# Performance work log

Hardware: AMD Instinct MI355X
Metric: run time of the kernel (lower is better)

Reference implementation:

```python
import jax, jax.numpy as jnp
import numpy as np

N, E = 50000, 800000
F, H, M = 64, 128, 64  # feature_dim, hidden_dim, message_dim (message_dim must equal feature_dim)


def _mlp(x, W1, b1, W2, b2):
    return jnp.maximum(x @ W1 + b1, 0.0) @ W2 + b2


def setup_inputs() -> dict:
    key = jax.random.key(0)
    ks = jax.random.split(key, 20)
    p = lambda k, s: (jax.random.normal(k, s, jnp.float32) * 0.05)
    return {
        "z_h": jax.random.normal(ks[0], (N, F), jnp.float32),
        "pos_world": jax.random.normal(ks[1], (3,), jnp.float32),
        "edge_index": jax.random.randint(ks[2], (2, E), 0, N),
        "We1": p(ks[3], (2 * F + 8, H)), "be1": p(ks[4], (H,)),
        "We2": p(ks[5], (H, M)), "be2": p(ks[6], (M,)),
        "Wg1": p(ks[7], (2 * F + 8, H)), "bg1": p(ks[8], (H,)),
        "Wg2": p(ks[9], (H, 1)), "bg2": p(ks[10], (1,)),
        "Wn1": p(ks[11], (F + M, H)), "bn1": p(ks[12], (H,)),
        "Wn2": p(ks[13], (H, F)), "bn2": p(ks[14], (F,)),
        "Ww1": p(ks[15], (F + 3, H)), "bw1": p(ks[16], (H,)),
        "Ww2": p(ks[17], (H, M)), "bw2": p(ks[18], (M,)),
    }


def reference(z_h, pos_world, edge_index,
              We1, be1, We2, be2,
              Wg1, bg1, Wg2, bg2,
              Wn1, bn1, Wn2, bn2,
              Ww1, bw1, Ww2, bw2):
    src, tgt = edge_index[0], edge_index[1]
    zs = z_h[src]  # [E, F]
    zt = z_h[tgt]  # [E, F]

    # edge features: diff(3) + dist(1) + vel cross product(3) + its norm(1)
    diff = zs[:, 0:3] - zt[:, 0:3]
    dist = jnp.sum(diff * diff, axis=-1, keepdims=True)
    cross = jnp.cross(zs[:, 3:6], zt[:, 3:6])
    cross_n = jnp.linalg.norm(cross, axis=-1, keepdims=True)
    e_feat = jnp.concatenate([diff, dist, cross, cross_n], axis=-1)  # [E, 8]

    inp_edge = jnp.concatenate([zs, zt, e_feat], axis=-1)  # [E, 2F+8]
    m = _mlp(inp_edge, We1, be1, We2, be2)                 # [E, M]
    w = jax.nn.sigmoid(_mlp(inp_edge, Wg1, bg1, Wg2, bg2))  # [E, 1]

    # scatter_add weighted messages to target nodes
    m_agg_h = jax.ops.segment_sum(w * m, tgt, num_segments=N)  # [N, F] (M == F)

    # world message: sum over all nodes, broadcast back
    diff_world = z_h[:, 0:3] - pos_world
    inp_world = jnp.concatenate([z_h, diff_world], axis=-1)  # [N, F+3]
    m_h_w = _mlp(inp_world, Ww1, bw1, Ww2, bw2)              # [N, M]
    m_agg_w = jnp.sum(m_h_w, axis=0, keepdims=True)          # [1, M] -> broadcast

    m_agg_total = m_agg_h + m_agg_w
    inp_node = jnp.concatenate([z_h, m_agg_total], axis=-1)  # [N, F+M]
    delta_z_h = _mlp(inp_node, Wn1, bn1, Wn2, bn2)           # [N, F]
    return delta_z_h
```

## Files before the change

### kernel.cpp

```cpp
#include <hip/hip_runtime.h>
#include <math.h>

#define NN 50000
#define NE 800000
#define EB 128
#define EBLOCKS (NE / EB)
#define WBLOCKS ((NN + 63) / 64)

typedef float     f32x4  __attribute__((ext_vector_type(4)));
typedef __bf16    bf16x8 __attribute__((ext_vector_type(8)));
typedef _Float16  f16x2  __attribute__((ext_vector_type(2)));
typedef _Float16  f16x8  __attribute__((ext_vector_type(8)));

#define WE1F_OFF 0
#define WE2F_OFF 5120
#define WN1F_OFF 6144
#define WN2F_OFF 8192
#define WW1F_OFF 9216
#define WW2F_OFF 10752
#define NCHUNKS  11776


__device__ inline bf16x8 pack8(float4 a, float4 b) {
    bf16x8 r;
    r[0] = (__bf16)a.x; r[1] = (__bf16)a.y; r[2] = (__bf16)a.z; r[3] = (__bf16)a.w;
    r[4] = (__bf16)b.x; r[5] = (__bf16)b.y; r[6] = (__bf16)b.z; r[7] = (__bf16)b.w;
    return r;
}

__device__ inline void pk_atomic_add_f16(void* addr, f16x2 v) {
#if __has_builtin(__builtin_amdgcn_global_atomic_fadd_v2f16)
    __builtin_amdgcn_global_atomic_fadd_v2f16((f16x2*)addr, v);
#else
    asm volatile("global_atomic_pk_add_f16 %0, %1, off"
                 :: "v"(addr), "v"(v) : "memory");
#endif
}

__global__ __launch_bounds__(256) void pack_weights(
    const float* __restrict__ We1, const float* __restrict__ Wg1,
    const float* __restrict__ We2, const float* __restrict__ Wn1,
    const float* __restrict__ Wn2, const float* __restrict__ Ww1,
    const float* __restrict__ Ww2, bf16x8* __restrict__ wsF)
{
    int c = blockIdx.x * 256 + threadIdx.x;
    if (c >= NCHUNKS) return;
    const int lane = c & 63, l16 = lane & 15, row8 = ((lane >> 4) & 3) * 8;
    bf16x8 p;
    if (c < WE2F_OFF) {
        int ct = (c >> 6) & 15, kc = c >> 10;
        int col = ct * 16 + l16;
        const float* src = (col < 128) ? (We1 + col) : (Wg1 + (col - 128));
#pragma unroll
        for (int i = 0; i < 8; i++) {
            int r = kc * 32 + row8 + i;
            p[i] = (__bf16)((r < 136) ? src[(size_t)r * 128] : 0.f);
        }
    } else if (c < WN1F_OFF) {
        int cc = c - WE2F_OFF; int ct = (cc >> 6) & 3, kc = cc >> 8;
        int col = ct * 16 + l16;
#pragma unroll
        for (int i = 0; i < 8; i++)
            p[i] = (__bf16)We2[(size_t)(kc * 32 + row8 + i) * 64 + col];
    } else if (c < WN2F_OFF) {
        int cc = c - WN1F_OFF; int ct = (cc >> 6) & 7, kc = cc >> 9;
        int col = ct * 16 + l16;
#pragma unroll
        for (int i = 0; i < 8; i++)
            p[i] = (__bf16)Wn1[(size_t)(kc * 32 + row8 + i) * 128 + col];
    } else if (c < WW1F_OFF) {
        int cc = c - WN2F_OFF; int ct = (cc >> 6) & 3, kc = cc >> 8;
        int col = ct * 16 + l16;
#pragma unroll
        for (int i = 0; i < 8; i++)
            p[i] = (__bf16)Wn2[(size_t)(kc * 32 + row8 + i) * 64 + col];
    } else if (c < WW2F_OFF) {
        int cc = c - WW1F_OFF; int ct = (cc >> 6) & 7, kc = cc >> 9;
        int col = ct * 16 + l16;
#pragma unroll
        for (int i = 0; i < 8; i++) {
            int r = kc * 32 + row8 + i;
            p[i] = (__bf16)((r < 67) ? Ww1[(size_t)r * 128 + col] : 0.f);
        }
    } else {
        int cc = c - WW2F_OFF; int ct = (cc >> 6) & 3, kc = cc >> 8;
        int col = ct * 16 + l16;
#pragma unroll
        for (int i = 0; i < 8; i++)
            p[i] = (__bf16)Ww2[(size_t)(kc * 32 + row8 + i) * 64 + col];
    }
    wsF[c] = p;
}

union FusedLds {
    bf16x8 XF[2560];
    struct {
        bf16x8   HF[2048];
        _Float16 M[EB * 68];
    } s;
};

__global__ __launch_bounds__(512, 4) void fused_kernel(
    const float* __restrict__ z_h, const int* __restrict__ ei,
    const bf16x8* __restrict__ We1F, const bf16x8* __restrict__ We2F,
    const float* __restrict__ be1, const float* __restrict__ be2,
    const float* __restrict__ bg1, const float* __restrict__ Wg2,
    const float* __restrict__ bg2,
    const float* __restrict__ pos_world,
    const bf16x8* __restrict__ Ww1F, const bf16x8* __restrict__ Ww2F,
    const float* __restrict__ bw1, const float* __restrict__ bw2,
    float* __restrict__ magg_rows,
    float* __restrict__ m_agg_w)
{
    __shared__ FusedLds U;
    __shared__ int   tgt_s[EB];
    __shared__ float gred[4][EB];
    __shared__ float wgt[EB];

    const int t = threadIdx.x;
    const int lane = t & 63, w = t >> 6;
    const int quad = lane >> 4, l16 = lane & 15;

    if (blockIdx.x >= EBLOCKS) {
        const int n0 = (blockIdx.x - EBLOCKS) * 64;
        {
            int nn = t >> 3, q = t & 7;
            int mt = nn >> 4, l16e = nn & 15;
            int node = n0 + nn; if (node >= NN) node = NN - 1;
            if (q < 4) {
                const float4* zr = (const float4*)(z_h + (long)node * 64) + q * 4;
                float4 a0 = zr[0], a1 = zr[1], a2 = zr[2], a3 = zr[3];
                int kcs = q >> 1, qa = (q & 1) * 2;
                U.XF[(kcs * 4 + mt) * 64 + qa * 16 + l16e]       = pack8(a0, a1);
                U.XF[(kcs * 4 + mt) * 64 + (qa + 1) * 16 + l16e] = pack8(a2, a3);
            } else if (q == 4) {
                float4 a0 = *(const float4*)(z_h + (long)node * 64);
                bf16x8 f;
#pragma unroll
                for (int i = 0; i < 8; i++) f[i] = (__bf16)0.f;
                f[0] = (__bf16)(a0.x - pos_world[0]);
                f[1] = (__bf16)(a0.y - pos_world[1]);
                f[2] = (__bf16)(a0.z - pos_world[2]);
                U.XF[(8 + mt) * 64 + l16e] = f;
            } else {
                bf16x8 z;
#pragma unroll
                for (int i = 0; i < 8; i++) z[i] = (__bf16)0.f;
                U.XF[(8 + mt) * 64 + (q - 4) * 16 + l16e] = z;
            }
        }
        __syncthreads();

        f32x4 acc[4];
        {
            float b = bw1[w * 16 + l16];
#pragma unroll
            for (int mt = 0; mt < 4; mt++) { f32x4 v = {b, b, b, b}; acc[mt] = v; }
        }
#pragma unroll
        for (int kc = 0; kc < 3; kc++) {
            bf16x8 bfr = Ww1F[(kc * 8 + w) * 64 + lane];
#pragma unroll
            for (int mt = 0; mt < 4; mt++)
                acc[mt] = __builtin_amdgcn_mfma_f32_16x16x32_bf16(
                    U.XF[(kc * 4 + mt) * 64 + lane], bfr, acc[mt], 0, 0, 0);
        }
        __syncthreads();

        {
            __bf16* HFp = (__bf16*)U.s.HF;
            int cw = w * 16 + l16;
            int kc2 = cw >> 5, quad2 = (cw >> 3) & 3, ii = cw & 7;
#pragma unroll
            for (int mt = 0; mt < 4; mt++)
#pragma unroll
                for (int r = 0; r < 4; r++)
                    HFp[(((kc2 * 4 + mt) * 64) + quad2 * 16 + quad * 4 + r) * 8 + ii] =
                        (__bf16)fmaxf(acc[mt][r], 0.f);
        }
        __syncthreads();

        {
            const int nt = w & 3, mh = w >> 2;
            f32x4 acc2[2];
            float b2 = bw2[nt * 16 + l16];
#pragma unroll
            for (int m = 0; m < 2; m++) { f32x4 v = {b2, b2, b2, b2}; acc2[m] = v; }
#pragma unroll
            for (int kc = 0; kc < 4; kc++) {
                bf16x8 b2f = Ww2F[(kc * 4 + nt) * 64 + lane];
#pragma unroll
                for (int m = 0; m < 2; m++)
                    acc2[m] = __builtin_amdgcn_mfma_f32_16x16x32_bf16(
                        U.s.HF[(kc * 4 + mh * 2 + m) * 64 + lane], b2f, acc2[m], 0, 0, 0);
            }
            float s = 0.f;
#pragma unroll
            for (int m = 0; m < 2; m++)
#pragma unroll
                for (int r = 0; r < 4; r++) {
                    int node = n0 + (mh * 2 + m) * 16 + quad * 4 + r;
                    s += (node < NN) ? acc2[m][r] : 0.f;
                }
            s += __shfl_xor(s, 16, 64);
            s += __shfl_xor(s, 32, 64);
            if (quad == 0) atomicAdd(m_agg_w + nt * 16 + l16, s);
        }
        return;
    }

    const int e0 = blockIdx.x * EB;

    {
        const int ee = t >> 2, sub = t & 3;
        const int mt = ee >> 4, l16e = ee & 15;
        const int eg = e0 + ee;
        const int rs = ei[eg], rt = ei[NE + eg];
        if (sub == 0) tgt_s[ee] = rt;
        const int qa = (sub & 1) * 2;
        const float4* zs = (const float4*)(z_h + (long)rs * 64) + sub * 4;
        float4 a0 = zs[0], a1 = zs[1], a2 = zs[2], a3 = zs[3];
        const float4* zt = (const float4*)(z_h + (long)rt * 64) + sub * 4;
        float4 b0 = zt[0], b1 = zt[1], b2 = zt[2], b3 = zt[3];
        const int kcs = (sub >> 1);
        U.XF[(kcs * 8 + mt) * 64 + qa * 16 + l16e]             = pack8(a0, a1);
        U.XF[(kcs * 8 + mt) * 64 + (qa + 1) * 16 + l16e]       = pack8(a2, a3);
        U.XF[((kcs + 2) * 8 + mt) * 64 + qa * 16 + l16e]       = pack8(b0, b1);
        U.XF[((kcs + 2) * 8 + mt) * 64 + (qa + 1) * 16 + l16e] = pack8(b2, b3);
        if (sub == 0) {
            float dx = a0.x - b0.x, dy = a0.y - b0.y, dz = a0.z - b0.z;
            float ax = a0.w, ay = a1.x, az = a1.y;
            float bx = b0.w, by = b1.x, bz = b1.y;
            float cx = ay * bz - az * by;
            float cy = az * bx - ax * bz;
            float cz = ax * by - ay * bx;
            bf16x8 f;
            f[0] = (__bf16)dx; f[1] = (__bf16)dy; f[2] = (__bf16)dz;
            f[3] = (__bf16)(dx * dx + dy * dy + dz * dz);
            f[4] = (__bf16)cx; f[5] = (__bf16)cy; f[6] = (__bf16)cz;
            f[7] = (__bf16)sqrtf(cx * cx + cy * cy + cz * cz);
            U.XF[(32 + mt) * 64 + l16e] = f;
        } else {
            bf16x8 z;
#pragma unroll
            for (int i = 0; i < 8; i++) z[i] = (__bf16)0.f;
            U.XF[(32 + mt) * 64 + sub * 16 + l16e] = z;
        }
    }
    __syncthreads();

    f32x4 acc[8][2];
#pragma unroll
    for (int nt = 0; nt < 2; nt++) {
        int col = (w * 2 + nt) * 16 + l16;
        float b = (col < 128) ? be1[col] : bg1[col - 128];
#pragma unroll
        for (int mt = 0; mt < 8; mt++) { f32x4 v = {b, b, b, b}; acc[mt][nt] = v; }
    }
    bf16x8 bcur0 = We1F[(w * 2) * 64 + lane];
    bf16x8 bcur1 = We1F[(w * 2 + 1) * 64 + lane];
#pragma unroll
    for (int kc = 0; kc < 5; kc++) {
        bf16x8 bnx0, bnx1;
        if (kc < 4) {
            bnx0 = We1F[((kc + 1) * 16 + w * 2) * 64 + lane];
            bnx1 = We1F[((kc + 1) * 16 + w * 2 + 1) * 64 + lane];
        }
#pragma unroll
        for (int mt = 0; mt < 8; mt++) {
            bf16x8 af = U.XF[(kc * 8 + mt) * 64 + lane];
            acc[mt][0] = __builtin_amdgcn_mfma_f32_16x16x32_bf16(af, bcur0, acc[mt][0], 0, 0, 0);
            acc[mt][1] = __builtin_amdgcn_mfma_f32_16x16x32_bf16(af, bcur1, acc[mt][1], 0, 0, 0);
        }
        bcur0 = bnx0; bcur1 = bnx1;
    }
    __syncthreads();

    if (w < 4) {
        __bf16* HFp = (__bf16*)U.s.HF;
#pragma unroll
        for (int nt = 0; nt < 2; nt++) {
            int cw = (w * 2 + nt) * 16 + l16;
            int kc2 = cw >> 5, quad2 = (cw >> 3) & 3, ii = cw & 7;
#pragma unroll
            for (int mt = 0; mt < 8; mt++)
#pragma unroll
                for (int r = 0; r < 4; r++)
                    HFp[(((kc2 * 8 + mt) * 64) + quad2 * 16 + quad * 4 + r) * 8 + ii] =
                        (__bf16)fmaxf(acc[mt][nt][r], 0.f);
        }
    } else {
        float gp[8][4];
#pragma unroll
        for (int mt = 0; mt < 8; mt++)
#pragma unroll
            for (int r = 0; r < 4; r++) gp[mt][r] = 0.f;
#pragma unroll
        for (int nt = 0; nt < 2; nt++) {
            float wg = Wg2[((w - 4) * 2 + nt) * 16 + l16];
#pragma unroll
            for (int mt = 0; mt < 8; mt++)
#pragma unroll
                for (int r = 0; r < 4; r++)
                    gp[mt][r] += fmaxf(acc[mt][nt][r], 0.f) * wg;
        }
#pragma unroll
        for (int mask = 1; mask < 16; mask <<= 1)
#pragma unroll
            for (int mt = 0; mt < 8; mt++)
#pragma unroll
                for (int r = 0; r < 4; r++)
                    gp[mt][r] += __shfl_xor(gp[mt][r], mask, 64);
        if (l16 == 0) {
#pragma unroll
            for (int mt = 0; mt < 8; mt++)
#pragma unroll
                for (int r = 0; r < 4; r++)
                    gred[w - 4][mt * 16 + quad * 4 + r] = gp[mt][r];
        }
    }
    __syncthreads();

    if (t < EB) {
        float g = bg2[0] + gred[0][t] + gred[1][t] + gred[2][t] + gred[3][t];
        wgt[t] = 1.f / (1.f + __expf(-g));
    }

    f32x4 acc2[8];
    if (w < 4) {
        float b2 = be2[w * 16 + l16];
#pragma unroll
        for (int mt = 0; mt < 8; mt++) { f32x4 v = {b2, b2, b2, b2}; acc2[mt] = v; }
        bf16x8 c2 = We2F[w * 64 + lane];
#pragma unroll
        for (int kc = 0; kc < 4; kc++) {
            bf16x8 n2;
            if (kc < 3) n2 = We2F[((kc + 1) * 4 + w) * 64 + lane];
#pragma unroll
            for (int mt = 0; mt < 8; mt++)
                acc2[mt] = __builtin_amdgcn_mfma_f32_16x16x32_bf16(
                    U.s.HF[(kc * 8 + mt) * 64 + lane], c2, acc2[mt], 0, 0, 0);
            c2 = n2;
        }
    }
    __syncthreads();

    if (w < 4) {
#pragma unroll
        for (int mt = 0; mt < 8; mt++)
#pragma unroll
            for (int r = 0; r < 4; r++) {
                int edge = mt * 16 + quad * 4 + r;
                U.s.M[edge * 68 + w * 16 + l16] =
                    (_Float16)(acc2[mt][r] * wgt[edge]);
            }
    }
    __syncthreads();

    {
        const int p = t & 31, eb = t >> 5;
        char* base = (char*)magg_rows;
#pragma unroll
        for (int k = 0; k < 8; k++) {
            int e = eb + k * 16;
            f16x2 v = *(const f16x2*)&U.s.M[e * 68 + p * 2];
            pk_atomic_add_f16(base + (long)tgt_s[e] * 256 + p * 4, v);
        }
    }
}

__global__ __launch_bounds__(512, 4) void node_kernel(
    const float* __restrict__ z_h,
    const float* __restrict__ m_agg_w,
    const bf16x8* __restrict__ Wn1F, const bf16x8* __restrict__ Wn2F,
    const float* __restrict__ bn1, const float* __restrict__ bn2,
    float* __restrict__ outp)
{
    __shared__ union { bf16x8 XF[1024]; bf16x8 HF[1024]; } U;
    const int t = threadIdx.x;
    const int n0 = blockIdx.x * 64;
    const int lane = t & 63, w = t >> 6;
    const int quad = lane >> 4, l16 = lane & 15;

    {
        int nn = t >> 3, q = t & 7;
        int mt = nn >> 4, l16e = nn & 15;
        int node = n0 + nn; if (node >= NN) node = NN - 1;
        int half = q >> 2, sub = q & 3;
        bf16x8 c0, c1;
        if (half == 0) {
            const float4* zr = (const float4*)(z_h + (long)node * 64) + sub * 4;
            c0 = pack8(zr[0], zr[1]);
            c1 = pack8(zr[2], zr[3]);
        } else {
            const f16x8* mr = (const f16x8*)((const char*)outp + (long)node * 256) + sub * 2;
            f16x8 r0 = mr[0], r1 = mr[1];
            const float* mw = m_agg_w + sub * 16;
#pragma unroll
            for (int i = 0; i < 8; i++) {
                c0[i] = (__bf16)((float)r0[i] + mw[i]);
                c1[i] = (__bf16)((float)r1[i] + mw[i + 8]);
            }
        }
        int kcs = (sub >> 1) + half * 2, qa = (sub & 1) * 2;
        U.XF[(kcs * 4 + mt) * 64 + qa * 16 + l16e]       = c0;
        U.XF[(kcs * 4 + mt) * 64 + (qa + 1) * 16 + l16e] = c1;
    }
    __syncthreads();

    f32x4 acc[4];
    {
        float b = bn1[w * 16 + l16];
#pragma unroll
        for (int mt = 0; mt < 4; mt++) { f32x4 v = {b, b, b, b}; acc[mt] = v; }
    }
#pragma unroll
    for (int kc = 0; kc < 4; kc++) {
        bf16x8 bfr = Wn1F[(kc * 8 + w) * 64 + lane];
#pragma unroll
        for (int mt = 0; mt < 4; mt++)
            acc[mt] = __builtin_amdgcn_mfma_f32_16x16x32_bf16(
                U.XF[(kc * 4 + mt) * 64 + lane], bfr, acc[mt], 0, 0, 0);
    }
    __syncthreads();

    {
        __bf16* HFp = (__bf16*)U.HF;
        int cw = w * 16 + l16;
        int kc2 = cw >> 5, quad2 = (cw >> 3) & 3, ii = cw & 7;
#pragma unroll
        for (int mt = 0; mt < 4; mt++)
#pragma unroll
            for (int r = 0; r < 4; r++)
                HFp[(((kc2 * 4 + mt) * 64) + quad2 * 16 + quad * 4 + r) * 8 + ii] =
                    (__bf16)fmaxf(acc[mt][r], 0.f);
    }
    __syncthreads();

    {
        const int nt = w & 3, mh = w >> 2;
        f32x4 acc2[2];
        float b2 = bn2[nt * 16 + l16];
#pragma unroll
        for (int m = 0; m < 2; m++) { f32x4 v = {b2, b2, b2, b2}; acc2[m] = v; }
#pragma unroll
        for (int kc = 0; kc < 4; kc++) {
            bf16x8 b2f = Wn2F[(kc * 4 + nt) * 64 + lane];
#pragma unroll
            for (int m = 0; m < 2; m++)
                acc2[m] = __builtin_amdgcn_mfma_f32_16x16x32_bf16(
                    U.HF[(kc * 4 + mh * 2 + m) * 64 + lane], b2f, acc2[m], 0, 0, 0);
        }
#pragma unroll
        for (int m = 0; m < 2; m++)
#pragma unroll
            for (int r = 0; r < 4; r++) {
                int node = n0 + (mh * 2 + m) * 16 + quad * 4 + r;
                if (node < NN)
                    outp[(long)node * 64 + nt * 16 + l16] = acc2[m][r];
            }
    }
}

extern "C" void kernel_launch(void* const* d_in, const int* in_sizes, int n_in,
                              void* d_out, int out_size, void* d_ws, size_t ws_size,
                              hipStream_t stream)
{
    const float* z_h       = (const float*)d_in[0];
    const float* pos_world = (const float*)d_in[1];
    const int*   ei        = (const int*)d_in[2];
    const float* We1 = (const float*)d_in[3];  const float* be1 = (const float*)d_in[4];
    const float* We2 = (const float*)d_in[5];  const float* be2 = (const float*)d_in[6];
    const float* Wg1 = (const float*)d_in[7];  const float* bg1 = (const float*)d_in[8];
    const float* Wg2 = (const float*)d_in[9];  const float* bg2 = (const float*)d_in[10];
    const float* Wn1 = (const float*)d_in[11]; const float* bn1 = (const float*)d_in[12];
    const float* Wn2 = (const float*)d_in[13]; const float* bn2 = (const float*)d_in[14];
    const float* Ww1 = (const float*)d_in[15]; const float* bw1 = (const float*)d_in[16];
    const float* Ww2 = (const float*)d_in[17]; const float* bw2 = (const float*)d_in[18];

    float*  outp    = (float*)d_out;
    float*  m_agg_w = (float*)d_ws;
    bf16x8* wsF     = (bf16x8*)((char*)d_ws + 256);

    hipMemsetAsync(d_out, 0, (size_t)NN * 64 * sizeof(float), stream);
    hipMemsetAsync(d_ws, 0, 256, stream);

    pack_weights<<<(NCHUNKS + 255) / 256, 256, 0, stream>>>(
        We1, Wg1, We2, Wn1, Wn2, Ww1, Ww2, wsF);
    fused_kernel<<<EBLOCKS + WBLOCKS, 512, 0, stream>>>(
        z_h, ei, wsF + WE1F_OFF, wsF + WE2F_OFF,
        be1, be2, bg1, Wg2, bg2,
        pos_world, wsF + WW1F_OFF, wsF + WW2F_OFF, bw1, bw2,
        outp, m_agg_w);
    node_kernel<<<(NN + 63) / 64, 512, 0, stream>>>(
        z_h, m_agg_w, wsF + WN1F_OFF, wsF + WN2F_OFF, bn1, bn2, outp);
}
```

Before: 296.8 us.

## Counting-sort edges by target and pre-reduce messages before atomic scatter

Adds histogram, single-block scan and scatter kernels that counting-sort edge ids by target node. The permutation is stored in the unused upper half of each output row. The edge kernel then processes edges in target order and sums consecutive same-target messages in registers within each 16-edge wave group, so it issues far fewer packed f16 global atomics. Target-row gathers also become more cache friendly. In exchange it adds three extra launches, including a serial single-block scan, plus 1.6M random integer atomics for the sort.

```diff
diff --git a/kernel.cpp b/kernel.cpp
--- a/kernel.cpp
+++ b/kernel.cpp
@@ -20,6 +20,11 @@
 #define WW2F_OFF 10752
 #define NCHUNKS  11776
 
+#define CNT_BASE NE
+
+__device__ inline int* slotp(void* base, int i) {
+    return (int*)((char*)base + (((long)(i >> 5)) << 8) + 128 + ((i & 31) << 2));
+}
 
 __device__ inline bf16x8 pack8(float4 a, float4 b) {
     bf16x8 r;
@@ -35,6 +40,47 @@
     asm volatile("global_atomic_pk_add_f16 %0, %1, off"
                  :: "v"(addr), "v"(v) : "memory");
 #endif
+}
+
+__global__ __launch_bounds__(512) void hist_kernel(
+    const int* __restrict__ ei, float* __restrict__ db)
+{
+    int e = blockIdx.x * 512 + threadIdx.x;
+    if (e >= NE) return;
+    atomicAdd(slotp(db, CNT_BASE + ei[NE + e]), 1);
+}
+
+__global__ __launch_bounds__(1024) void scan_kernel(float* __restrict__ db)
+{
+    __shared__ int ps[1024];
+    const int i = threadIdx.x;
+    int s = 0;
+    for (int j = 0; j < 49; j++) s += *slotp(db, CNT_BASE + i * 49 + j);
+    ps[i] = s;
+    __syncthreads();
+    for (int off = 1; off < 1024; off <<= 1) {
+        int v = (i >= off) ? ps[i - off] : 0;
+        __syncthreads();
+        ps[i] += v;
+        __syncthreads();
+    }
+    int run = ps[i] - s;
+    for (int j = 0; j < 49; j++) {
+        int* p = slotp(db, CNT_BASE + i * 49 + j);
+        int c = *p;
+        *p = run;
+        run += c;
+    }
+}
+
+__global__ __launch_bounds__(512) void scat_kernel(
+    const int* __restrict__ ei, float* __restrict__ db)
+{
+    int e = blockIdx.x * 512 + threadIdx.x;
+    if (e >= NE) return;
+    int t = ei[NE + e];
+    int pos = atomicAdd(slotp(db, CNT_BASE + t), 1);
+    *slotp(db, pos) = e;
 }
 
 __global__ __launch_bounds__(256) void pack_weights(
@@ -214,7 +260,7 @@
     {
         const int ee = t >> 2, sub = t & 3;
         const int mt = ee >> 4, l16e = ee & 15;
-        const int eg = e0 + ee;
+        const int eg = *slotp(magg_rows, e0 + ee);
         const int rs = ei[eg], rt = ei[NE + eg];
         if (sub == 0) tgt_s[ee] = rt;
         const int qa = (sub & 1) * 2;
@@ -358,13 +404,23 @@
     __syncthreads();
 
     {
-        const int p = t & 31, eb = t >> 5;
+        const int c = lane;
         char* base = (char*)magg_rows;
-#pragma unroll
-        for (int k = 0; k < 8; k++) {
-            int e = eb + k * 16;
-            f16x2 v = *(const f16x2*)&U.s.M[e * 68 + p * 2];
-            pk_atomic_add_f16(base + (long)tgt_s[e] * 256 + p * 4, v);
+        float acc3 = 0.f;
+#pragma unroll
+        for (int k = 0; k < 16; k++) {
+            int e = w * 16 + k;
+            acc3 += (float)U.s.M[e * 68 + c];
+            int cur = tgt_s[e];
+            bool fl = (k == 15) || (tgt_s[e + 1] != cur);
+            if (fl) {
+                float pr = __shfl_xor(acc3, 1, 64);
+                if (!(c & 1)) {
+                    f16x2 v; v[0] = (_Float16)acc3; v[1] = (_Float16)pr;
+                    pk_atomic_add_f16(base + (long)cur * 256 + c * 2, v);
+                }
+                acc3 = 0.f;
+            }
         }
     }
 }
@@ -487,6 +543,9 @@
 
     pack_weights<<<(NCHUNKS + 255) / 256, 256, 0, stream>>>(
         We1, Wg1, We2, Wn1, Wn2, Ww1, Ww2, wsF);
+    hist_kernel<<<(NE + 511) / 512, 512, 0, stream>>>(ei, outp);
+    scan_kernel<<<1, 1024, 0, stream>>>(outp);
+    scat_kernel<<<(NE + 511) / 512, 512, 0, stream>>>(ei, outp);
     fused_kernel<<<EBLOCKS + WBLOCKS, 512, 0, stream>>>(
         z_h, ei, wsF + WE1F_OFF, wsF + WE2F_OFF,
         be1, be2, bg1, Wg2, bg2,
```

Result: slower. 468.3 us (+57.8%).
